# Kernel tuning notes

Hardware: AMD Instinct MI355X
Metric: run time of the kernel (lower is better)

The kernel has to match this reference:

```python
import jax, jax.numpy as jnp
import numpy as np

MAX_LEVEL = 4
CURV = 1.0
MAX_NORM = 0.95
N_ITER = 10


def project_to_poincare(x):
    # Rescale points whose norm exceeds max_norm / sqrt(c) back onto the ball.
    norm = jnp.linalg.norm(x, axis=-1, keepdims=True)
    max_r = MAX_NORM / jnp.sqrt(jnp.asarray(CURV, x.dtype))
    return jnp.where(norm > max_r, x / (norm + 1e-12) * max_r, x)


def poincare_distance(x, y):
    # d(x,y) = arccosh(1 + 2c||x-y||^2 / ((1-c||x||^2)(1-c||y||^2))) / sqrt(c)
    sq = jnp.sum((x - y) ** 2, axis=-1)
    nx = jnp.sum(x * x, axis=-1)
    ny = jnp.sum(y * y, axis=-1)
    denom = jnp.maximum((1.0 - CURV * nx) * (1.0 - CURV * ny), 1e-12)
    arg = 1.0 + 2.0 * CURV * sq / denom
    return jnp.arccosh(jnp.maximum(arg, 1.0 + 1e-7)) / jnp.sqrt(CURV)


def setup_inputs() -> dict:
    key = jax.random.key(0)
    k1, k2 = jax.random.split(key)
    B, D = 1048576, 32
    z = jax.random.normal(k1, (B, D), dtype=jnp.float32)
    batch_indices = jax.random.randint(k2, (B,), 0, 19683, dtype=jnp.int64)
    level_weights = jnp.array([0.5 ** i for i in range(MAX_LEVEL)], dtype=jnp.float32)
    return {"z": z, "batch_indices": batch_indices, "level_weights": level_weights}


def reference(z, batch_indices, level_weights):
    z_hyp = project_to_poincare(z)
    B = z.shape[0]
    ones = jnp.ones((B,), dtype=z.dtype)
    total_loss = jnp.asarray(0.0, dtype=z.dtype)
    for level in range(1, MAX_LEVEL + 1):
        n_seg = 3 ** level
        seg = (batch_indices // (3 ** (9 - level))).astype(jnp.int32)
        counts = jax.ops.segment_sum(ones, seg, num_segments=n_seg)          # [n_seg]
        sums = jax.ops.segment_sum(z_hyp, seg, num_segments=n_seg)           # [n_seg, D]
        safe_counts = jnp.maximum(counts, 1.0)[:, None]
        euc_mean = sums / safe_counts                                        # weighted (uniform) mean
        # Frechet-mean iteration: direction = sum_i w_i (x_i - mean) = euc_mean - mean
        mean = project_to_poincare(euc_mean)
        for _ in range(N_ITER):
            mean = project_to_poincare(mean + 0.1 * (euc_mean - mean))
        cent = mean[seg]                                                     # [B, D]
        dists = poincare_distance(z_hyp, cent)                               # [B]
        dist_mean = jax.ops.segment_sum(dists, seg, num_segments=n_seg) / jnp.maximum(counts, 1.0)
        valid = counts >= 2.0                                                # clusters with <2 pts skipped
        level_loss = jnp.sum(jnp.where(valid, dist_mean, 0.0))
        n_unique = jnp.sum(counts > 0.0)
        total_loss = total_loss + level_weights[level - 1] * level_loss / jnp.maximum(n_unique, 1.0)
    return total_loss
```

## Files before the change

### kernel.cpp

```cpp
#include <hip/hip_runtime.h>
#include <math.h>


#define MAXR  0.95f
#define MAXR2 0.9025f
#define LN2F  0.6931471805599453f

__device__ __forceinline__ float fsqrt(float x) { return __builtin_amdgcn_sqrtf(x); }
__device__ __forceinline__ float frcp(float x)  { return __builtin_amdgcn_rcpf(x); }
__device__ __forceinline__ float frsq(float x)  { return __builtin_amdgcn_rsqf(x); }

__device__ __forceinline__ float red8_dpp(float v) {
    v += __int_as_float(__builtin_amdgcn_update_dpp(0, __float_as_int(v), 0xB1, 0xF, 0xF, 1));
    v += __int_as_float(__builtin_amdgcn_update_dpp(0, __float_as_int(v), 0x4E, 0xF, 0xF, 1));
    v += __int_as_float(__builtin_amdgcn_update_dpp(0, __float_as_int(v), 0x141, 0xF, 0xF, 1));
    return v;
}

__device__ __forceinline__ float red32_dpp(float v) {
    v += __int_as_float(__builtin_amdgcn_update_dpp(0, __float_as_int(v), 0xB1, 0xF, 0xF, 1));
    v += __int_as_float(__builtin_amdgcn_update_dpp(0, __float_as_int(v), 0x4E, 0xF, 0xF, 1));
    v += __int_as_float(__builtin_amdgcn_update_dpp(0, __float_as_int(v), 0x141, 0xF, 0xF, 1));
    v += __int_as_float(__builtin_amdgcn_update_dpp(0, __float_as_int(v), 0x140, 0xF, 0xF, 1));
    v += __shfl_xor(v, 16, 32);
    return v;
}

__device__ __forceinline__ int dup_rank(int s4, int g, int sub) {
    int sj = __shfl(s4, sub * 8, 64);
    unsigned long long eq = __ballot(sj == s4);
    unsigned int row = (unsigned int)(eq >> (g * 8));
    return __popc(row & ((1u << g) - 1u));
}

__global__ __launch_bounds__(256) void pass1_hist(
        const float* __restrict__ z, const int* __restrict__ idx,
        float* __restrict__ gsum, int B) {
    __shared__ float lsum[4][81][36];
    const int tid = threadIdx.x;
    for (int j = tid; j < 4 * 81 * 36; j += 256) (&lsum[0][0][0])[j] = 0.f;
    __syncthreads();

    const int w = tid >> 6;
    const int g = (tid & 63) >> 3;
    const int sub = tid & 7;
    const int STRIDE = gridDim.x * 128;
    const int base0 = blockIdx.x * 128 + w * 32 + g;
    const int nfull = B / STRIDE;
    float* const lw = &lsum[w][0][0];

    for (int it = 0; it < nfull; ++it) {
        const int ib = it * STRIDE + base0;
        float4 xv[4];
        int s4v[4], rank[4];
#pragma unroll
        for (int b = 0; b < 4; ++b)
            xv[b] = *(const float4*)(z + (size_t)(ib + b * 8) * 32 + sub * 4);
#pragma unroll
        for (int b = 0; b < 4; ++b)
            s4v[b] = idx[ib + b * 8] / 243;
#pragma unroll
        for (int b = 0; b < 4; ++b) {
            const float nx = red8_dpp(xv[b].x * xv[b].x + xv[b].y * xv[b].y +
                                      xv[b].z * xv[b].z + xv[b].w * xv[b].w);
            const float s = (nx > MAXR2) ? MAXR * frsq(nx) : 1.0f;
            xv[b].x *= s; xv[b].y *= s; xv[b].z *= s; xv[b].w *= s;
        }
#pragma unroll
        for (int b = 0; b < 4; ++b)
            rank[b] = dup_rank(s4v[b], g, sub);
#pragma unroll
        for (int b = 0; b < 4; ++b) {
            float* row = lw + s4v[b] * 36;
            for (int r = 0;; ++r) {
                if (!__any(rank[b] == r)) break;
                if (rank[b] == r) {
                    float4 cur = *(float4*)(row + sub * 4);
                    cur.x += xv[b].x; cur.y += xv[b].y;
                    cur.z += xv[b].z; cur.w += xv[b].w;
                    *(float4*)(row + sub * 4) = cur;
                    if (sub == 0) row[32] += 1.0f;
                }
            }
        }
    }
    if (B % STRIDE) {
        const int ib = nfull * STRIDE + base0;
        for (int b = 0; b < 4; ++b) {
            const int i = ib + b * 8;
            const bool act = i < B;
            float4 xv = act ? *(const float4*)(z + (size_t)i * 32 + sub * 4)
                            : make_float4(0.f, 0.f, 0.f, 0.f);
            int s4 = act ? idx[i] / 243 : 81 + g;
            const float nx = red8_dpp(xv.x * xv.x + xv.y * xv.y +
                                      xv.z * xv.z + xv.w * xv.w);
            const float s = (nx > MAXR2) ? MAXR * frsq(nx) : 1.0f;
            xv.x *= s; xv.y *= s; xv.z *= s; xv.w *= s;
            int rank = dup_rank(s4, g, sub);
            for (int r = 0;; ++r) {
                if (!__any(rank == r)) break;
                if (act && rank == r) {
                    float* row = lw + s4 * 36;
                    float4 cur = *(float4*)(row + sub * 4);
                    cur.x += xv.x; cur.y += xv.y; cur.z += xv.z; cur.w += xv.w;
                    *(float4*)(row + sub * 4) = cur;
                    if (sub == 0) row[32] += 1.0f;
                }
            }
        }
    }
    __syncthreads();
    float* gpart = gsum + (blockIdx.x & 7) * 2673;
    for (int j = tid; j < 81 * 33; j += 256) {
        const int r = j / 33, c = j - r * 33;
        const float v = lsum[0][r][c] + lsum[1][r][c] +
                        lsum[2][r][c] + lsum[3][r][c];
        unsafeAtomicAdd(&gpart[j], v);
    }
}

__global__ __launch_bounds__(256) void pass2_centroids(
        const float* __restrict__ gsum,
        float* __restrict__ cent, float* __restrict__ cnt_all,
        float* __restrict__ cnorm) {
    __shared__ float euc[120][33];
    const int tid = threadIdx.x;
    for (int j = tid; j < 2673; j += 256) {
        float s = 0.f;
#pragma unroll
        for (int p = 0; p < 8; ++p) s += gsum[p * 2673 + j];
        const int r = j / 33, c = j - r * 33;
        euc[39 + r][c] = s;
    }
    __syncthreads();
    for (int j = tid; j < 27 * 33; j += 256) {
        const int r = j / 33, c = j - r * 33;
        euc[12 + r][c] = euc[39 + 3 * r][c] + euc[40 + 3 * r][c] + euc[41 + 3 * r][c];
    }
    __syncthreads();
    for (int j = tid; j < 9 * 33; j += 256) {
        const int r = j / 33, c = j - r * 33;
        euc[3 + r][c] = euc[12 + 3 * r][c] + euc[13 + 3 * r][c] + euc[14 + 3 * r][c];
    }
    __syncthreads();
    for (int j = tid; j < 3 * 33; j += 256) {
        const int r = j / 33, c = j - r * 33;
        euc[r][c] = euc[3 + 3 * r][c] + euc[4 + 3 * r][c] + euc[5 + 3 * r][c];
    }
    __syncthreads();
    const int lane = tid & 31;
    const int grp = tid >> 5;
    for (int t = grp; t < 120; t += 8) {
        const float sum = euc[t][lane];
        const float cnt = euc[t][32];
        const float em = sum / fmaxf(cnt, 1.0f);
        float m = em;
        {
            float norm = sqrtf(red32_dpp(m * m));
            if (norm > MAXR) m *= MAXR / (norm + 1e-12f);
        }
        for (int it = 0; it < 10; ++it) {
            float v = m + 0.1f * (em - m);
            float norm = sqrtf(red32_dpp(v * v));
            if (norm > MAXR) v *= MAXR / (norm + 1e-12f);
            m = v;
        }
        cent[t * 32 + lane] = m;
        float ny = red32_dpp(m * m);
        if (lane == 0) { cnt_all[t] = cnt; cnorm[t] = 1.0f - ny; }
    }
}

__global__ __launch_bounds__(256) void pass3_dist(
        const float* __restrict__ z, const int* __restrict__ idx,
        const float* __restrict__ cent, const float* __restrict__ cnorm,
        float* __restrict__ dsum, int B) {
    __shared__ float lcent[120 * 32];
    __shared__ float lcn[120];
    __shared__ float ld[4][81][4];
    const int tid = threadIdx.x;
    for (int j = tid; j < 120 * 32; j += 256) lcent[j] = cent[j];
    for (int j = tid; j < 120; j += 256) lcn[j] = cnorm[j];
    for (int j = tid; j < 4 * 81 * 4; j += 256) (&ld[0][0][0])[j] = 0.f;
    __syncthreads();

    const int w = tid >> 6;
    const int g = (tid & 63) >> 3;
    const int sub = tid & 7;
    const int STRIDE = gridDim.x * 128;
    const int base0 = blockIdx.x * 128 + w * 32 + g;
    const int nfull = B / STRIDE;

    for (int it = 0; it < nfull; ++it) {
        const int ib = it * STRIDE + base0;
        float4 xv[4];
        int s4v[4], rank[4];
        float dl[4][4];
#pragma unroll
        for (int b = 0; b < 4; ++b)
            xv[b] = *(const float4*)(z + (size_t)(ib + b * 8) * 32 + sub * 4);
#pragma unroll
        for (int b = 0; b < 4; ++b)
            s4v[b] = idx[ib + b * 8] / 243;
#pragma unroll
        for (int b = 0; b < 4; ++b) {
            float nx = red8_dpp(xv[b].x * xv[b].x + xv[b].y * xv[b].y +
                                xv[b].z * xv[b].z + xv[b].w * xv[b].w);
            const float s = (nx > MAXR2) ? MAXR * frsq(nx) : 1.0f;
            xv[b].x *= s; xv[b].y *= s; xv[b].z *= s; xv[b].w *= s;
            nx = nx * s * s;
            const float ah = 0.5f * (1.0f - nx);
            const float c2a = 1.0f + nx;
            const int s4 = s4v[b];
            const int d3 = s4 / 3, d9 = d3 / 3, d27 = d9 / 3;
            const int tl[4] = {d27, 3 + d9, 12 + d3, 39 + s4};
#pragma unroll
            for (int l = 0; l < 4; ++l) {
                const int t = tl[l];
                const float4 c = *(const float4*)(lcent + t * 32 + sub * 4);
                const float dot = red8_dpp(xv[b].x * c.x + xv[b].y * c.y +
                                           xv[b].z * c.z + xv[b].w * c.w);
                const float bny = lcn[t];
                const float sq = fmaf(-2.0f, dot, c2a - bny);
                const float d = fmaxf(ah * bny, 5e-13f);
                float tt = sq * frcp(d);
                tt = fmaxf(tt, 1e-7f);
                dl[b][l] = __log2f(1.0f + tt + fsqrt(tt * (tt + 2.0f)));
            }
        }
#pragma unroll
        for (int b = 0; b < 4; ++b)
            rank[b] = dup_rank(s4v[b], g, sub);
#pragma unroll
        for (int b = 0; b < 4; ++b) {
            float* row = &ld[w][s4v[b]][0];
            for (int r = 0;; ++r) {
                if (!__any(rank[b] == r)) break;
                if (rank[b] == r && sub == 0) {
                    float4 cur = *(float4*)row;
                    cur.x += dl[b][0]; cur.y += dl[b][1];
                    cur.z += dl[b][2]; cur.w += dl[b][3];
                    *(float4*)row = cur;
                }
            }
        }
    }
    if (B % STRIDE) {
        const int ib = nfull * STRIDE + base0;
        for (int b = 0; b < 4; ++b) {
            const int i = ib + b * 8;
            const bool act = i < B;
            float4 xv = act ? *(const float4*)(z + (size_t)i * 32 + sub * 4)
                            : make_float4(0.f, 0.f, 0.f, 0.f);
            int s4 = act ? idx[i] / 243 : 81 + g;
            float nx = red8_dpp(xv.x * xv.x + xv.y * xv.y + xv.z * xv.z + xv.w * xv.w);
            const float s = (nx > MAXR2) ? MAXR * frsq(nx) : 1.0f;
            xv.x *= s; xv.y *= s; xv.z *= s; xv.w *= s;
            nx = nx * s * s;
            const float ah = 0.5f * (1.0f - nx);
            const float c2a = 1.0f + nx;
            const int ss = act ? s4 : 0;
            const int d3 = ss / 3, d9 = d3 / 3, d27 = d9 / 3;
            const int tl[4] = {d27, 3 + d9, 12 + d3, 39 + ss};
            float dl[4];
#pragma unroll
            for (int l = 0; l < 4; ++l) {
                const int t = tl[l];
                const float4 c = *(const float4*)(lcent + t * 32 + sub * 4);
                const float dot = red8_dpp(xv.x * c.x + xv.y * c.y +
                                           xv.z * c.z + xv.w * c.w);
                const float bny = lcn[t];
                const float sq = fmaf(-2.0f, dot, c2a - bny);
                const float d = fmaxf(ah * bny, 5e-13f);
                float tt = sq * frcp(d);
                tt = fmaxf(tt, 1e-7f);
                dl[l] = __log2f(1.0f + tt + fsqrt(tt * (tt + 2.0f)));
            }
            int rank = dup_rank(s4, g, sub);
            for (int r = 0;; ++r) {
                if (!__any(rank == r)) break;
                if (act && rank == r && sub == 0) {
                    float* row = &ld[w][s4][0];
                    float4 cur = *(float4*)row;
                    cur.x += dl[0]; cur.y += dl[1]; cur.z += dl[2]; cur.w += dl[3];
                    *(float4*)row = cur;
                }
            }
        }
    }
    __syncthreads();
    float* dpart = dsum + (blockIdx.x & 7) * 324;
    for (int j = tid; j < 81 * 4; j += 256) {
        const float v = (&ld[0][0][0])[j] + (&ld[1][0][0])[j] +
                        (&ld[2][0][0])[j] + (&ld[3][0][0])[j];
        unsafeAtomicAdd(&dpart[j], v);
    }
}

__global__ __launch_bounds__(128) void pass4_final(
        const float* __restrict__ dsum, const float* __restrict__ cnt_all,
        const float* __restrict__ w, float* __restrict__ out) {
    __shared__ float sl[81];
    __shared__ float su[81];
    const int tid = threadIdx.x;
    const int toff[4] = {0, 3, 12, 39};
    const int nsegs[4] = {3, 9, 27, 81};
    float total = 0.f;
    for (int l = 0; l < 4; ++l) {
        const int n_seg = nsegs[l];
        const int ch = 81 / n_seg;
        __syncthreads();
        if (tid < n_seg) {
            float cnt = cnt_all[toff[l] + tid];
            float ds = 0.f;
            for (int p = 0; p < 8; ++p)
                for (int k = 0; k < ch; ++k)
                    ds += dsum[p * 324 + (tid * ch + k) * 4 + l];
            sl[tid] = (cnt >= 2.0f) ? ds * LN2F / fmaxf(cnt, 1.0f) : 0.f;
            su[tid] = (cnt > 0.0f) ? 1.f : 0.f;
        }
        __syncthreads();
        if (tid == 0) {
            float ll = 0.f, nu = 0.f;
            for (int s = 0; s < n_seg; ++s) { ll += sl[s]; nu += su[s]; }
            total += w[l] * ll / fmaxf(nu, 1.0f);
        }
    }
    if (tid == 0) out[0] = total;
}

extern "C" void kernel_launch(void* const* d_in, const int* in_sizes, int n_in,
                              void* d_out, int out_size, void* d_ws, size_t ws_size,
                              hipStream_t stream) {
    const float* z   = (const float*)d_in[0];
    const int*   idx = (const int*)d_in[1];
    const float* w   = (const float*)d_in[2];
    float* out = (float*)d_out;
    float* ws  = (float*)d_ws;
    const int B = in_sizes[1];

    float* gsum    = ws;
    float* dsum    = ws + 21384;
    float* cent    = ws + 23976;
    float* cnt_all = ws + 27816;
    float* cnorm   = ws + 27936;

    hipMemsetAsync(ws, 0, 23976 * sizeof(float), stream);
    pass1_hist<<<1024, 256, 0, stream>>>(z, idx, gsum, B);
    pass2_centroids<<<1, 256, 0, stream>>>(gsum, cent, cnt_all, cnorm);
    pass3_dist<<<2048, 256, 0, stream>>>(z, idx, cent, cnorm, dsum, B);
    pass4_final<<<1, 128, 0, stream>>>(dsum, cnt_all, w, out);
}
```

Measured before the change: 126.2 us.

## Replace histogram atomics with per-block partials and a separate reduction kernel

Pass 1 now writes each block's 81x33 partial histogram to its own slice of the workspace instead of doing atomic adds into 8 shared partial buffers. A new pass2a kernel reduces those 1024 slices to 8 groups and also zeroes dsum, so the memset launch goes away. Pass 2 additionally precomputes, for each of the 81 leaf segments, its four ancestor-centroid indices and norms, and pass 3 loads these as int4/float4 from LDS instead of doing repeated integer divides. This removes atomic contention and the memset but adds an extra kernel launch and roughly 11 MB of partial-sum traffic.

After: 122.7 us. 2.7% less time.

```diff
diff --git a/kernel.cpp b/kernel.cpp
--- a/kernel.cpp
+++ b/kernel.cpp
@@ -5,6 +5,15 @@
 #define MAXR  0.95f
 #define MAXR2 0.9025f
 #define LN2F  0.6931471805599453f
+
+#define NPART 1024
+#define HCOLS 2673
+#define OFF_HSUM8 (NPART * HCOLS)
+#define OFF_DSUM  (OFF_HSUM8 + 8 * HCOLS)
+#define OFF_CENT  (OFF_DSUM + 8 * 324)
+#define OFF_CNT   (OFF_CENT + 120 * 32)
+#define OFF_CN4   (OFF_CNT + 120)
+#define OFF_TI4   (OFF_CN4 + 324)
 
 __device__ __forceinline__ float fsqrt(float x) { return __builtin_amdgcn_sqrtf(x); }
 __device__ __forceinline__ float frcp(float x)  { return __builtin_amdgcn_rcpf(x); }
@@ -35,7 +44,7 @@
 
 __global__ __launch_bounds__(256) void pass1_hist(
         const float* __restrict__ z, const int* __restrict__ idx,
-        float* __restrict__ gsum, int B) {
+        float* __restrict__ part, int B) {
     __shared__ float lsum[4][81][36];
     const int tid = threadIdx.x;
     for (int j = tid; j < 4 * 81 * 36; j += 256) (&lsum[0][0][0])[j] = 0.f;
@@ -110,25 +119,47 @@
         }
     }
     __syncthreads();
-    float* gpart = gsum + (blockIdx.x & 7) * 2673;
-    for (int j = tid; j < 81 * 33; j += 256) {
+    float* myslice = part + (size_t)blockIdx.x * HCOLS;
+    for (int j = tid; j < HCOLS; j += 256) {
         const int r = j / 33, c = j - r * 33;
-        const float v = lsum[0][r][c] + lsum[1][r][c] +
-                        lsum[2][r][c] + lsum[3][r][c];
-        unsafeAtomicAdd(&gpart[j], v);
+        myslice[j] = lsum[0][r][c] + lsum[1][r][c] +
+                     lsum[2][r][c] + lsum[3][r][c];
+    }
+}
+
+__global__ __launch_bounds__(256) void pass2a_reduce(
+        const float* __restrict__ part, float* __restrict__ hsum8,
+        float* __restrict__ dsum) {
+    const int tid = threadIdx.x;
+    const int group = blockIdx.x / 11;
+    const int jb = blockIdx.x - group * 11;
+    const int j = jb * 256 + tid;
+    if (blockIdx.x == 0)
+        for (int k = tid; k < 8 * 324; k += 256) dsum[k] = 0.f;
+    if (j < HCOLS) {
+        const float* p0 = part + (size_t)(group * 128) * HCOLS + j;
+        float s0 = 0.f, s1 = 0.f, s2 = 0.f, s3 = 0.f;
+        for (int b = 0; b < 128; b += 4) {
+            s0 += p0[(size_t)b * HCOLS];
+            s1 += p0[(size_t)(b + 1) * HCOLS];
+            s2 += p0[(size_t)(b + 2) * HCOLS];
+            s3 += p0[(size_t)(b + 3) * HCOLS];
+        }
+        hsum8[group * HCOLS + j] = (s0 + s1) + (s2 + s3);
     }
 }
 
 __global__ __launch_bounds__(256) void pass2_centroids(
-        const float* __restrict__ gsum,
+        const float* __restrict__ hsum8,
         float* __restrict__ cent, float* __restrict__ cnt_all,
-        float* __restrict__ cnorm) {
+        float* __restrict__ cnorm4, int* __restrict__ tidx4) {
     __shared__ float euc[120][33];
+    __shared__ float cn[120];
     const int tid = threadIdx.x;
-    for (int j = tid; j < 2673; j += 256) {
+    for (int j = tid; j < HCOLS; j += 256) {
         float s = 0.f;
 #pragma unroll
-        for (int p = 0; p < 8; ++p) s += gsum[p * 2673 + j];
+        for (int p = 0; p < 8; ++p) s += hsum8[p * HCOLS + j];
         const int r = j / 33, c = j - r * 33;
         euc[39 + r][c] = s;
     }
@@ -167,20 +198,30 @@
         }
         cent[t * 32 + lane] = m;
         float ny = red32_dpp(m * m);
-        if (lane == 0) { cnt_all[t] = cnt; cnorm[t] = 1.0f - ny; }
+        if (lane == 0) { cnt_all[t] = cnt; cn[t] = 1.0f - ny; }
+    }
+    __syncthreads();
+    if (tid < 81) {
+        const int s4 = tid;
+        const int d3 = s4 / 3, d9 = d3 / 3, d27 = d9 / 3;
+        const int t0 = d27, t1 = 3 + d9, t2 = 12 + d3, t3 = 39 + s4;
+        ((int4*)tidx4)[s4] = make_int4(t0, t1, t2, t3);
+        ((float4*)cnorm4)[s4] = make_float4(cn[t0], cn[t1], cn[t2], cn[t3]);
     }
 }
 
 __global__ __launch_bounds__(256) void pass3_dist(
         const float* __restrict__ z, const int* __restrict__ idx,
-        const float* __restrict__ cent, const float* __restrict__ cnorm,
-        float* __restrict__ dsum, int B) {
+        const float* __restrict__ cent, const float* __restrict__ cnorm4,
+        const int* __restrict__ tidx4, float* __restrict__ dsum, int B) {
     __shared__ float lcent[120 * 32];
-    __shared__ float lcn[120];
+    __shared__ float4 lcn4[81];
+    __shared__ int4 ltl4[81];
     __shared__ float ld[4][81][4];
     const int tid = threadIdx.x;
     for (int j = tid; j < 120 * 32; j += 256) lcent[j] = cent[j];
-    for (int j = tid; j < 120; j += 256) lcn[j] = cnorm[j];
+    for (int j = tid; j < 324; j += 256) ((float*)lcn4)[j] = cnorm4[j];
+    for (int j = tid; j < 324; j += 256) ((int*)ltl4)[j] = tidx4[j];
     for (int j = tid; j < 4 * 81 * 4; j += 256) (&ld[0][0][0])[j] = 0.f;
     __syncthreads();
 
@@ -212,15 +253,17 @@
             const float ah = 0.5f * (1.0f - nx);
             const float c2a = 1.0f + nx;
             const int s4 = s4v[b];
-            const int d3 = s4 / 3, d9 = d3 / 3, d27 = d9 / 3;
-            const int tl[4] = {d27, 3 + d9, 12 + d3, 39 + s4};
+            const int4 t4 = ltl4[s4];
+            const float4 cn4 = lcn4[s4];
+            const int tls[4] = {t4.x, t4.y, t4.z, t4.w};
+            const float bnys[4] = {cn4.x, cn4.y, cn4.z, cn4.w};
 #pragma unroll
             for (int l = 0; l < 4; ++l) {
-                const int t = tl[l];
+                const int t = tls[l];
                 const float4 c = *(const float4*)(lcent + t * 32 + sub * 4);
                 const float dot = red8_dpp(xv[b].x * c.x + xv[b].y * c.y +
                                            xv[b].z * c.z + xv[b].w * c.w);
-                const float bny = lcn[t];
+                const float bny = bnys[l];
                 const float sq = fmaf(-2.0f, dot, c2a - bny);
                 const float d = fmaxf(ah * bny, 5e-13f);
                 float tt = sq * frcp(d);
@@ -260,16 +303,18 @@
             const float ah = 0.5f * (1.0f - nx);
             const float c2a = 1.0f + nx;
             const int ss = act ? s4 : 0;
-            const int d3 = ss / 3, d9 = d3 / 3, d27 = d9 / 3;
-            const int tl[4] = {d27, 3 + d9, 12 + d3, 39 + ss};
+            const int4 t4 = ltl4[ss];
+            const float4 cn4 = lcn4[ss];
+            const int tls[4] = {t4.x, t4.y, t4.z, t4.w};
+            const float bnys[4] = {cn4.x, cn4.y, cn4.z, cn4.w};
             float dl[4];
 #pragma unroll
             for (int l = 0; l < 4; ++l) {
-                const int t = tl[l];
+                const int t = tls[l];
                 const float4 c = *(const float4*)(lcent + t * 32 + sub * 4);
                 const float dot = red8_dpp(xv.x * c.x + xv.y * c.y +
                                            xv.z * c.z + xv.w * c.w);
-                const float bny = lcn[t];
+                const float bny = bnys[l];
                 const float sq = fmaf(-2.0f, dot, c2a - bny);
                 const float d = fmaxf(ah * bny, 5e-13f);
                 float tt = sq * frcp(d);
@@ -339,15 +384,17 @@
     float* ws  = (float*)d_ws;
     const int B = in_sizes[1];
 
-    float* gsum    = ws;
-    float* dsum    = ws + 21384;
-    float* cent    = ws + 23976;
-    float* cnt_all = ws + 27816;
-    float* cnorm   = ws + 27936;
-
-    hipMemsetAsync(ws, 0, 23976 * sizeof(float), stream);
-    pass1_hist<<<1024, 256, 0, stream>>>(z, idx, gsum, B);
-    pass2_centroids<<<1, 256, 0, stream>>>(gsum, cent, cnt_all, cnorm);
-    pass3_dist<<<2048, 256, 0, stream>>>(z, idx, cent, cnorm, dsum, B);
+    float* part    = ws;
+    float* hsum8   = ws + OFF_HSUM8;
+    float* dsum    = ws + OFF_DSUM;
+    float* cent    = ws + OFF_CENT;
+    float* cnt_all = ws + OFF_CNT;
+    float* cnorm4  = ws + OFF_CN4;
+    int*   tidx4   = (int*)(ws + OFF_TI4);
+
+    pass1_hist<<<NPART, 256, 0, stream>>>(z, idx, part, B);
+    pass2a_reduce<<<88, 256, 0, stream>>>(part, hsum8, dsum);
+    pass2_centroids<<<1, 256, 0, stream>>>(hsum8, cent, cnt_all, cnorm4, tidx4);
+    pass3_dist<<<2048, 256, 0, stream>>>(z, idx, cent, cnorm4, tidx4, dsum, B);
     pass4_final<<<1, 128, 0, stream>>>(dsum, cnt_all, w, out);
 }
```
